# Optimization experiments

Hardware: AMD Instinct MI355X
Metric: run time of the kernel (lower is better)

The kernel has to match this reference:

```python
import jax, jax.numpy as jnp
import numpy as np

NEG = -1e30

def setup_inputs() -> dict:
    key = jax.random.key(0)
    ks = jax.random.split(key, 6)
    B, H, Lc, Lq = 32, 256, 1024, 256
    C = jax.random.normal(ks[0], (B, H, Lc), dtype=jnp.float32)
    Q = jax.random.normal(ks[1], (B, H, Lq), dtype=jnp.float32)
    cmask = jnp.ones((B, Lc), dtype=jnp.int32)
    qmask = jnp.ones((B, Lq), dtype=jnp.int32)
    # xavier_uniform on [3H,1]: bound = sqrt(6/(3H+1))
    bound = float(np.sqrt(6.0 / (3 * H + 1)))
    w = jax.random.uniform(ks[2], (3 * H,), minval=-bound, maxval=bound, dtype=jnp.float32)
    # kaiming_normal (relu, fan_in=4H): std = sqrt(2/(4H))
    W_res = jax.random.normal(ks[3], (H, 4 * H), dtype=jnp.float32) * float(np.sqrt(2.0 / (4 * H)))
    b_res = jnp.zeros((H,), dtype=jnp.float32)
    return {"C": C, "Q": Q, "cmask": cmask, "qmask": qmask, "w": w, "W_res": W_res, "b_res": b_res}

def reference(C, Q, cmask, qmask, w, W_res, b_res):
    H = w.shape[0] // 3
    Ct = jnp.transpose(C, (0, 2, 1))  # [B, Lc, H]
    Qt = jnp.transpose(Q, (0, 2, 1))  # [B, Lq, H]
    w1, w2, w3 = w[:H], w[H:2 * H], w[2 * H:]
    # trilinear similarity S[b,i,j] = Ct_i.w1 + Qt_j.w2 + (Ct_i*Qt_j).w3
    S = (jnp.einsum('blh,h->bl', Ct, w1)[:, :, None]
         + jnp.einsum('bmh,h->bm', Qt, w2)[:, None, :]
         + jnp.einsum('blh,bmh->blm', Ct * w3, Qt))  # [B, Lc, Lq]
    qm = qmask.astype(jnp.float32)[:, None, :]  # [B,1,Lq]
    cm = cmask.astype(jnp.float32)[:, :, None]  # [B,Lc,1]
    S_row = jax.nn.softmax(S + NEG * (1.0 - qm), axis=2)   # over questions
    S_col = jax.nn.softmax(S + NEG * (1.0 - cm), axis=1)   # over context
    A = jnp.einsum('blm,bmh->blh', S_row, Qt)  # [B, Lc, H]
    Bm = jnp.einsum('blm,bkm->blk', S_row, S_col)  # [B, Lc, Lc]
    Bv = jnp.einsum('blk,bkh->blh', Bm, Ct)  # [B, Lc, H]
    cat = jnp.concatenate([Ct, A, Ct * A, Ct * Bv], axis=2)  # [B, Lc, 4H]
    out = jax.nn.relu(jnp.einsum('blf,hf->blh', cat, W_res) + b_res)
    return jnp.transpose(out, (0, 2, 1))  # [B, H, Lc]
```

## Files before the change

### kernel.cpp

```cpp
#include <hip/hip_runtime.h>
#include <math.h>

#define NB 32
#define NH 256
#define NLC 1024
#define NLQ 256
#define NEGV (-1e30f)
#define LCHUNK 16
#define KSPLIT 4

typedef short short8 __attribute__((ext_vector_type(8)));
typedef float f32x4 __attribute__((ext_vector_type(4)));

__device__ inline short bf16_of(float f) {
  union { float f; unsigned u; } v;
  v.f = f;
  unsigned r = (v.u + 0x7fffu + ((v.u >> 16) & 1u)) >> 16;
  return (short)r;
}
__device__ inline float f_of(short s) {
  union { unsigned u; float f; } v;
  v.u = ((unsigned)(unsigned short)s) << 16;
  return v.f;
}
__device__ inline short8 cvt8(float4 a, float4 b) {
  short8 o;
  o[0] = bf16_of(a.x); o[1] = bf16_of(a.y); o[2] = bf16_of(a.z); o[3] = bf16_of(a.w);
  o[4] = bf16_of(b.x); o[5] = bf16_of(b.y); o[6] = bf16_of(b.z); o[7] = bf16_of(b.w);
  return o;
}

__device__ inline void lds_w8(short* lds, int r, int c, short8 v) {
  int byteoff = (r << 6) + (((c ^ ((r >> 1) & 3)) & 3) << 4);
  *(short8*)((char*)lds + byteoff) = v;
}
__device__ inline short8 lds_r8(const short* lds, int R, int g) {
  int byteoff = (R << 6) + (((g ^ ((R >> 1) & 3)) & 3) << 4);
  return *(const short8*)((const char*)lds + byteoff);
}
__device__ inline void stage_g(const short* src, int ld, short* lds, int t) {
  int L = t & 63, w = t >> 6;
  int cp = (L & 3) ^ ((L >> 3) & 3);
#pragma unroll
  for (int i = 0; i < 2; ++i) {
    int seg = w + i * 4;
    const short* g = src + (size_t)(seg * 16 + (L >> 2)) * ld + cp * 8;
    __builtin_amdgcn_global_load_lds(
        (const __attribute__((address_space(1))) unsigned int*)g,
        (__attribute__((address_space(3))) unsigned int*)(lds + seg * 512), 16,
        0, 0);
  }
}

#define GEMM_IDS                                       \
  int t = threadIdx.x, lane = t & 63, w = t >> 6;      \
  int ln = lane & 15, g = lane >> 4;                   \
  int wr = (w >> 1) << 6, wc = (w & 1) << 6;           \
  (void)wr; (void)wc;

#define MFMA_STEP(AS, BS)                                                      \
  {                                                                            \
    short8 af[4], bfr[4];                                                      \
    _Pragma("unroll") for (int mi = 0; mi < 4; ++mi) af[mi] =                  \
        lds_r8(AS, wr + mi * 16 + ln, g);                                      \
    _Pragma("unroll") for (int ni = 0; ni < 4; ++ni) bfr[ni] =                 \
        lds_r8(BS, wc + ni * 16 + ln, g);                                      \
    _Pragma("unroll") for (int mi = 0; mi < 4; ++mi)                           \
        _Pragma("unroll") for (int ni = 0; ni < 4; ++ni) acc[mi][ni] =         \
            __builtin_amdgcn_mfma_f32_16x16x32_bf16(af[mi], bfr[ni],           \
                                                    acc[mi][ni], 0, 0, 0);     \
  }

__global__ __launch_bounds__(256) void k_prep_c(const float* __restrict__ C,
                                                const float* __restrict__ w,
                                                short* __restrict__ Ct_lh,
                                                float* __restrict__ s1p) {
  __shared__ float Ts[64][65];
  __shared__ float red[4][64];
  int b = blockIdx.z, h0 = blockIdx.y << 6, l0 = blockIdx.x << 6;
  int t = threadIdx.x;
  int hr = t >> 4, lc = (t & 15) << 2;
  const float* Cb = C + ((size_t)b * NH + h0) * NLC + l0;
#pragma unroll
  for (int i = 0; i < 4; ++i) {
    float4 v = *(const float4*)&Cb[(size_t)(hr + i * 16) * NLC + lc];
    Ts[hr + i * 16][lc + 0] = v.x;
    Ts[hr + i * 16][lc + 1] = v.y;
    Ts[hr + i * 16][lc + 2] = v.z;
    Ts[hr + i * 16][lc + 3] = v.w;
  }
  __syncthreads();
  int lr = t >> 2, hc = (t & 3) << 4;
  short* dst = &Ct_lh[((size_t)b * NLC + l0 + lr) * NH + h0 + hc];
  short8 o0, o1;
#pragma unroll
  for (int j = 0; j < 8; ++j) o0[j] = bf16_of(Ts[hc + j][lr]);
#pragma unroll
  for (int j = 0; j < 8; ++j) o1[j] = bf16_of(Ts[hc + 8 + j][lr]);
  *(short8*)dst = o0;
  *(short8*)(dst + 8) = o1;
  int q = t >> 6, lq = t & 63;
  float a = 0.f;
#pragma unroll
  for (int j = 0; j < 16; ++j) a += Ts[(q << 4) + j][lq] * w[h0 + (q << 4) + j];
  red[q][lq] = a;
  __syncthreads();
  if (q == 0)
    s1p[((size_t)blockIdx.y * NB + b) * NLC + l0 + lq] =
        red[0][lq] + red[1][lq] + red[2][lq] + red[3][lq];
}

__global__ __launch_bounds__(256) void k_prep_q(const float* __restrict__ Q,
                                                const float* __restrict__ w,
                                                short* __restrict__ Qtw3,
                                                short* __restrict__ Qb_hm,
                                                float* __restrict__ s2p) {
  __shared__ float Ts[64][65];
  __shared__ float red[4][64];
  int b = blockIdx.z, h0 = blockIdx.y << 6, m0 = blockIdx.x << 6;
  int t = threadIdx.x;
  int hr = t >> 4, mc = (t & 15) << 2;
  const float* w3 = w + 2 * NH;
  const float* Qb = Q + ((size_t)b * NH + h0) * NLQ + m0;
#pragma unroll
  for (int i = 0; i < 4; ++i) {
    int h = hr + i * 16;
    float w3v = w3[h0 + h];
    float4 v = *(const float4*)&Qb[(size_t)h * NLQ + mc];
    short4 qb;
    qb.x = bf16_of(v.x); qb.y = bf16_of(v.y);
    qb.z = bf16_of(v.z); qb.w = bf16_of(v.w);
    *(short4*)&Qb_hm[((size_t)b * NH + h0 + h) * NLQ + m0 + mc] = qb;
    Ts[h][mc + 0] = v.x * w3v;
    Ts[h][mc + 1] = v.y * w3v;
    Ts[h][mc + 2] = v.z * w3v;
    Ts[h][mc + 3] = v.w * w3v;
  }
  __syncthreads();
  int mr = t >> 2, hc = (t & 3) << 4;
  short* dst = &Qtw3[((size_t)b * NLQ + m0 + mr) * NH + h0 + hc];
  short8 o0, o1;
#pragma unroll
  for (int j = 0; j < 8; ++j) o0[j] = bf16_of(Ts[hc + j][mr]);
#pragma unroll
  for (int j = 0; j < 8; ++j) o1[j] = bf16_of(Ts[hc + 8 + j][mr]);
  *(short8*)dst = o0;
  *(short8*)(dst + 8) = o1;
  int q = t >> 6, mq = t & 63;
  const float* w2 = w + NH;
  float a = 0.f;
#pragma unroll
  for (int j = 0; j < 16; ++j) {
    int h = (q << 4) + j;
    a += Qb[(size_t)h * NLQ + mq] * w2[h0 + h];
  }
  red[q][mq] = a;
  __syncthreads();
  if (q == 0)
    s2p[((size_t)blockIdx.y * NB + b) * NLQ + m0 + mq] =
        red[0][mq] + red[1][mq] + red[2][mq] + red[3][mq];
}

__global__ __launch_bounds__(256) void k_sfin(const float* __restrict__ s1p,
                                              const float* __restrict__ s2p,
                                              float* __restrict__ s1,
                                              float* __restrict__ s2) {
  int i = blockIdx.x * 256 + threadIdx.x;
  const int N1 = NB * NLC, N2 = NB * NLQ;
  if (i < N1) {
    s1[i] = s1p[i] + s1p[N1 + i] + s1p[2 * N1 + i] + s1p[3 * N1 + i];
  } else {
    int j = i - N1;
    s2[j] = s2p[j] + s2p[N2 + j] + s2p[2 * N2 + j] + s2p[3 * N2 + j];
  }
}

__global__ __launch_bounds__(256) void k_prep_bf16(const float* __restrict__ X,
                                                   short* __restrict__ Y) {
  size_t i = ((size_t)blockIdx.x * 256 + threadIdx.x) * 8;
  float4 v0 = *(const float4*)&X[i];
  float4 v1 = *(const float4*)&X[i + 4];
  *(short8*)&Y[i] = cvt8(v0, v1);
}

__global__ __launch_bounds__(256) void k_sgemm(
    const short* __restrict__ Ct_lh, const short* __restrict__ Qtw3,
    const float* __restrict__ s1, const float* __restrict__ s2,
    float* __restrict__ S) {
  __shared__ short As[2][4096], Bs[2][4096];
  int b = blockIdx.z, l0 = blockIdx.y << 7, m0 = blockIdx.x << 7;
  GEMM_IDS
  const short* Ag = Ct_lh + ((size_t)b * NLC + l0) * NH;
  const short* Bg = Qtw3 + ((size_t)b * NLQ + m0) * NH;
  f32x4 acc[4][4] = {};
  stage_g(Ag, NH, As[0], t);
  stage_g(Bg, NH, Bs[0], t);
  __syncthreads();
  int cur = 0;
  for (int kn = 32; kn <= NH; kn += 32) {
    if (kn < NH) {
      stage_g(Ag + kn, NH, As[cur ^ 1], t);
      stage_g(Bg + kn, NH, Bs[cur ^ 1], t);
    }
    MFMA_STEP(As[cur], Bs[cur])
    __syncthreads();
    cur ^= 1;
  }
#pragma unroll
  for (int mi = 0; mi < 4; ++mi)
#pragma unroll
    for (int ni = 0; ni < 4; ++ni)
#pragma unroll
      for (int r = 0; r < 4; ++r) {
        int l = l0 + wr + mi * 16 + g * 4 + r;
        int m = m0 + wc + ni * 16 + ln;
        S[((size_t)b * NLC + l) * NLQ + m] =
            acc[mi][ni][r] + s1[b * NLC + l] + s2[b * NLQ + m];
      }
}

__global__ __launch_bounds__(256) void k_colpart(const float* __restrict__ S,
                                                 const int* __restrict__ cmask,
                                                 float* __restrict__ pmax,
                                                 float* __restrict__ psum) {
  int idx = blockIdx.x;
  int chunk = idx & (LCHUNK - 1);
  int mb = (idx >> 4) & 3;
  int b = idx >> 6;
  int m0 = mb << 6;
  int tx = threadIdx.x & 63, ty = threadIdx.x >> 6;
  const float* Sb = S + (size_t)b * NLC * NLQ + (size_t)(chunk * 64) * NLQ;
  const int* cm = cmask + b * NLC + chunk * 64;
  float mx = -INFINITY, sm = 0.f;
#pragma unroll 4
  for (int l = ty; l < 64; l += 4) {
    float x = Sb[(size_t)l * NLQ + m0 + tx] + (cm[l] ? 0.f : NEGV);
    float nmx = fmaxf(mx, x);
    sm = sm * expf(mx - nmx) + expf(x - nmx);
    mx = nmx;
  }
  __shared__ float smx[4][64], ssm[4][64];
  smx[ty][tx] = mx;
  ssm[ty][tx] = sm;
  __syncthreads();
  if (ty == 0) {
#pragma unroll
    for (int r = 1; r < 4; ++r) {
      float m2 = smx[r][tx], s2 = ssm[r][tx];
      float nm = fmaxf(mx, m2);
      sm = sm * expf(mx - nm) + s2 * expf(m2 - nm);
      mx = nm;
    }
    int m = (b << 8) + m0 + tx;
    pmax[(size_t)m * LCHUNK + chunk] = mx;
    psum[(size_t)m * LCHUNK + chunk] = sm;
  }
}

__global__ __launch_bounds__(256) void k_colfin(const float* __restrict__ pmax,
                                                const float* __restrict__ psum,
                                                float* __restrict__ cmax,
                                                float* __restrict__ cinv) {
  int m = blockIdx.x * 256 + threadIdx.x;
  const float* pm = pmax + (size_t)m * LCHUNK;
  const float* ps = psum + (size_t)m * LCHUNK;
  float mx = pm[0], sm = ps[0];
#pragma unroll
  for (int c = 1; c < LCHUNK; ++c) {
    float m2 = pm[c], s2 = ps[c];
    float nm = fmaxf(mx, m2);
    sm = sm * expf(mx - nm) + s2 * expf(m2 - nm);
    mx = nm;
  }
  cmax[m] = mx;
  cinv[m] = 1.0f / sm;
}

__global__ __launch_bounds__(256) void k_rowsoft(float* __restrict__ S,
                                                 const int* __restrict__ qmask,
                                                 const int* __restrict__ cmask,
                                                 const float* __restrict__ cmax,
                                                 const float* __restrict__ cinv) {
  int wave = threadIdx.x >> 6, lane = threadIdx.x & 63;
  int idx = (blockIdx.x << 2) + wave;
  int b = idx >> 10;
  float* row = S + (size_t)idx * NLQ;
  const int* qm = qmask + b * NLQ;
  int m4 = lane << 2;
  float4 v = *(const float4*)&row[m4];
  int4 q = *(const int4*)&qm[m4];
  float x0 = v.x + (q.x ? 0.f : NEGV);
  float x1 = v.y + (q.y ? 0.f : NEGV);
  float x2 = v.z + (q.z ? 0.f : NEGV);
  float x3 = v.w + (q.w ? 0.f : NEGV);
  float mx = fmaxf(fmaxf(x0, x1), fmaxf(x2, x3));
#pragma unroll
  for (int off = 32; off > 0; off >>= 1) mx = fmaxf(mx, __shfl_xor(mx, off));
  float p0 = expf(x0 - mx), p1 = expf(x1 - mx);
  float p2 = expf(x2 - mx), p3 = expf(x3 - mx);
  float sm = p0 + p1 + p2 + p3;
#pragma unroll
  for (int off = 32; off > 0; off >>= 1) sm += __shfl_xor(sm, off);
  float iv = 1.0f / sm;
  short4 o;
  o.x = bf16_of(p0 * iv);
  o.y = bf16_of(p1 * iv);
  o.z = bf16_of(p2 * iv);
  o.w = bf16_of(p3 * iv);
  float cmf = (float)cmask[idx];
  float4 cm4 = *(const float4*)&cmax[(b << 8) + m4];
  float4 ci4 = *(const float4*)&cinv[(b << 8) + m4];
  short4 oc;
  oc.x = bf16_of(expf(v.x - cm4.x) * ci4.x * cmf);
  oc.y = bf16_of(expf(v.y - cm4.y) * ci4.y * cmf);
  oc.z = bf16_of(expf(v.z - cm4.z) * ci4.z * cmf);
  oc.w = bf16_of(expf(v.w - cm4.w) * ci4.w * cmf);
  *(short4*)((short*)row + m4) = o;
  *(short4*)((short*)row + 256 + m4) = oc;
}

__global__ __launch_bounds__(256) void k_tgemm(const float* __restrict__ C,
                                               const short* __restrict__ PcolS,
                                               float* __restrict__ Tp) {
  __shared__ short As[4096], Bs[4096];
  int b = blockIdx.z;
  int ks = blockIdx.y;
  int h0 = (blockIdx.x & 1) << 7;
  int m0 = (blockIdx.x >> 1) << 7;
  GEMM_IDS
  const float* Cb = C + ((size_t)b * NH + h0) * NLC;
  const short* Pb = PcolS + (size_t)b * NLC * 512 + 256 + m0;
  f32x4 acc[4][4] = {};
  int kbeg = ks * (NLC / KSPLIT), kend = kbeg + NLC / KSPLIT;
  int ca = lane & 3;
  int lloc = t >> 3, g2 = lloc >> 3, kin = lloc & 7;
  int mbase = (t & 7) << 4;
  for (int k0 = kbeg; k0 < kend; k0 += 32) {
    __syncthreads();
    {
#pragma unroll
      for (int i = 0; i < 2; ++i) {
        int seg = w + i * 4, r = seg * 16 + (lane >> 2);
        const float* src = &Cb[(size_t)r * NLC + k0 + ca * 8];
        float4 v0 = *(const float4*)src;
        float4 v1 = *(const float4*)(src + 4);
        lds_w8(As, r, ca, cvt8(v0, v1));
      }
    }
    {
      const short* srow = Pb + (size_t)(k0 + lloc) * 512;
      short8 x0 = *(const short8*)&srow[mbase];
      short8 x1 = *(const short8*)&srow[mbase + 8];
#pragma unroll
      for (int j = 0; j < 8; ++j) {
        int R = mbase + j;
        int byteoff =
            (R << 6) + (((g2 ^ ((R >> 1) & 3)) & 3) << 4) + (kin << 1);
        *(short*)((char*)Bs + byteoff) = x0[j];
      }
#pragma unroll
      for (int j = 0; j < 8; ++j) {
        int R = mbase + 8 + j;
        int byteoff =
            (R << 6) + (((g2 ^ ((R >> 1) & 3)) & 3) << 4) + (kin << 1);
        *(short*)((char*)Bs + byteoff) = x1[j];
      }
    }
    __syncthreads();
    MFMA_STEP(As, Bs)
  }
  float* dst = Tp + ((size_t)ks * NB + b) * NH * NLQ;
#pragma unroll
  for (int mi = 0; mi < 4; ++mi)
#pragma unroll
    for (int ni = 0; ni < 4; ++ni)
#pragma unroll
      for (int r = 0; r < 4; ++r) {
        int h = h0 + wr + mi * 16 + g * 4 + r;
        int m = m0 + wc + ni * 16 + ln;
        dst[(size_t)h * NLQ + m] = acc[mi][ni][r];
      }
}

__global__ __launch_bounds__(256) void k_tfin(const float* __restrict__ Tp,
                                              short* __restrict__ Tt) {
  size_t i = ((size_t)blockIdx.x * 256 + threadIdx.x) * 4;
  const size_t stride = (size_t)NB * NH * NLQ;
  float4 s = *(const float4*)&Tp[i];
#pragma unroll
  for (int ks = 1; ks < KSPLIT; ++ks) {
    float4 v = *(const float4*)&Tp[i + ks * stride];
    s.x += v.x; s.y += v.y; s.z += v.z; s.w += v.w;
  }
  short4 o;
  o.x = bf16_of(s.x);
  o.y = bf16_of(s.y);
  o.z = bf16_of(s.z);
  o.w = bf16_of(s.w);
  *(short4*)&Tt[i] = o;
}

__global__ __launch_bounds__(256) void k_abgemm(
    const short* __restrict__ Prow, const short* __restrict__ Qb_hm,
    const short* __restrict__ Tt, const short* __restrict__ Ct_lh,
    short* __restrict__ A_lh, short* __restrict__ CtBv_lh) {
  __shared__ short As[2][4096], Bs[2][4096];
  int b = blockIdx.z, l0 = blockIdx.y << 7, nb = blockIdx.x;
  GEMM_IDS
  const short* Ag = Prow + ((size_t)b * NLC + l0) * 512;
  const short* Bbase = (nb < 2)
                           ? Qb_hm + ((size_t)b * NH + nb * 128) * NLQ
                           : Tt + ((size_t)b * NH + (nb - 2) * 128) * NLQ;
  f32x4 acc[4][4] = {};
  stage_g(Ag, 512, As[0], t);
  stage_g(Bbase, NLQ, Bs[0], t);
  __syncthreads();
  int cur = 0;
  for (int kn = 32; kn <= NLQ; kn += 32) {
    if (kn < NLQ) {
      stage_g(Ag + kn, 512, As[cur ^ 1], t);
      stage_g(Bbase + kn, NLQ, Bs[cur ^ 1], t);
    }
    MFMA_STEP(As[cur], Bs[cur])
    __syncthreads();
    cur ^= 1;
  }
  int hbase = (nb & 1) << 7;
  if (nb < 2) {
#pragma unroll
    for (int mi = 0; mi < 4; ++mi)
#pragma unroll
      for (int ni = 0; ni < 4; ++ni)
#pragma unroll
        for (int r = 0; r < 4; ++r) {
          int l = l0 + wr + mi * 16 + g * 4 + r;
          int h = hbase + wc + ni * 16 + ln;
          A_lh[((size_t)b * NLC + l) * NH + h] = bf16_of(acc[mi][ni][r]);
        }
  } else {
#pragma unroll
    for (int mi = 0; mi < 4; ++mi)
#pragma unroll
      for (int ni = 0; ni < 4; ++ni)
#pragma unroll
        for (int r = 0; r < 4; ++r) {
          int l = l0 + wr + mi * 16 + g * 4 + r;
          int h = hbase + wc + ni * 16 + ln;
          size_t off = ((size_t)b * NLC + l) * NH + h;
          CtBv_lh[off] = bf16_of(f_of(Ct_lh[off]) * acc[mi][ni][r]);
        }
  }
}

__global__ __launch_bounds__(256) void k_out(
    const short* __restrict__ Wb, const short* __restrict__ Ct_lh,
    const short* __restrict__ A_lh, const short* __restrict__ CtBv_lh,
    const float* __restrict__ br, float* __restrict__ out) {
  __shared__ short As[2][4096], Bs[2][4096];
  int b = blockIdx.z, h0 = blockIdx.y << 7, l0 = blockIdx.x << 7;
  GEMM_IDS
  const short* Wg = Wb + (size_t)h0 * (4 * NH);
  size_t boff = ((size_t)b * NLC + l0) * NH;
  f32x4 acc[4][4] = {};
  stage_g(Wg, 4 * NH, As[0], t);
  stage_g(Ct_lh + boff, NH, Bs[0], t);
  __syncthreads();
  int cur = 0;
  for (int kn = 32; kn <= 4 * NH; kn += 32) {
    bool has = kn < 4 * NH;
    int regn = kn >> 8, kon = kn & 255;
    short8 x1[2], x2[2];
    int ca = lane & 3;
    if (has) {
      stage_g(Wg + kn, 4 * NH, As[cur ^ 1], t);
      if (regn != 2) {
        const short* base = (regn == 0) ? Ct_lh : (regn == 1) ? A_lh : CtBv_lh;
        stage_g(base + boff + kon, NH, Bs[cur ^ 1], t);
      } else {
#pragma unroll
        for (int i = 0; i < 2; ++i) {
          int seg = w + i * 4, r = seg * 16 + (lane >> 2);
          size_t off = boff + (size_t)r * NH + kon + ca * 8;
          x1[i] = *(const short8*)&Ct_lh[off];
          x2[i] = *(const short8*)&A_lh[off];
        }
      }
    }
    MFMA_STEP(As[cur], Bs[cur])
    if (has && regn == 2) {
#pragma unroll
      for (int i = 0; i < 2; ++i) {
        int seg = w + i * 4, r = seg * 16 + (lane >> 2);
        short8 o;
#pragma unroll
        for (int j = 0; j < 8; ++j)
          o[j] = bf16_of(f_of(x1[i][j]) * f_of(x2[i][j]));
        lds_w8(Bs[cur ^ 1], r, ca, o);
      }
    }
    __syncthreads();
    cur ^= 1;
  }
#pragma unroll
  for (int mi = 0; mi < 4; ++mi)
#pragma unroll
    for (int ni = 0; ni < 4; ++ni) {
      int h = h0 + wr + mi * 16 + g * 4;
      int l = l0 + wc + ni * 16 + ln;
#pragma unroll
      for (int r = 0; r < 4; ++r) {
        float bias = br[h + r];
        out[((size_t)b * NH + h + r) * NLC + l] =
            fmaxf(acc[mi][ni][r] + bias, 0.f);
      }
    }
}

extern "C" void kernel_launch(void* const* d_in, const int* in_sizes, int n_in,
                              void* d_out, int out_size, void* d_ws,
                              size_t ws_size, hipStream_t stream) {
  (void)in_sizes;
  (void)n_in;
  (void)out_size;
  (void)ws_size;
  const float* C = (const float*)d_in[0];
  const float* Q = (const float*)d_in[1];
  const int* cmask = (const int*)d_in[2];
  const int* qmask = (const int*)d_in[3];
  const float* w = (const float*)d_in[4];
  const float* W = (const float*)d_in[5];
  const float* br = (const float*)d_in[6];
  float* out = (float*)d_out;

  char* p = (char*)d_ws;
  float* S = (float*)p;       p += (size_t)NB * NLC * NLQ * 4;
  short* Ct_lh = (short*)p;   p += (size_t)NB * NLC * NH * 2;
  short* A_lh = (short*)p;    p += (size_t)NB * NLC * NH * 2;
  short* CtBv_lh = (short*)p; p += (size_t)NB * NLC * NH * 2;
  short* Tt = (short*)p;      p += (size_t)NB * NH * NLQ * 2;
  short* Qtw3 = (short*)p;    p += (size_t)NB * NLQ * NH * 2;
  short* Qb_hm = (short*)p;   p += (size_t)NB * NH * NLQ * 2;
  short* Wb = (short*)p;      p += (size_t)NH * 4 * NH * 2;
  float* s1 = (float*)p;      p += (size_t)NB * NLC * 4;
  float* s2 = (float*)p;      p += (size_t)NB * NLQ * 4;
  float* cmax = (float*)p;    p += (size_t)NB * NLQ * 4;
  float* cinv = (float*)p;    p += (size_t)NB * NLQ * 4;
  float* pmax = (float*)p;    p += (size_t)NB * NLQ * LCHUNK * 4;
  float* psum = (float*)p;    p += (size_t)NB * NLQ * LCHUNK * 4;
  float* s1p = (float*)p;     p += (size_t)4 * NB * NLC * 4;
  float* s2p = (float*)p;     p += (size_t)4 * NB * NLQ * 4;
  float* Tp = (float*)A_lh;
  short* Prow = (short*)S;

  k_prep_c<<<dim3(NLC / 64, NH / 64, NB), dim3(256), 0, stream>>>(C, w, Ct_lh,
                                                                  s1p);
  k_prep_q<<<dim3(NLQ / 64, NH / 64, NB), dim3(256), 0, stream>>>(
      Q, w, Qtw3, Qb_hm, s2p);
  k_prep_bf16<<<dim3(NH * 4 * NH / 2048), dim3(256), 0, stream>>>(W, Wb);
  k_sfin<<<dim3((NB * NLC + NB * NLQ) / 256), dim3(256), 0, stream>>>(
      s1p, s2p, s1, s2);
  k_sgemm<<<dim3(NLQ / 128, NLC / 128, NB), dim3(256), 0, stream>>>(
      Ct_lh, Qtw3, s1, s2, S);
  k_colpart<<<dim3(NB * 4 * LCHUNK), dim3(256), 0, stream>>>(S, cmask, pmax,
                                                             psum);
  k_colfin<<<dim3(NB * NLQ / 256), dim3(256), 0, stream>>>(pmax, psum, cmax,
                                                           cinv);
  k_rowsoft<<<dim3(NB * NLC / 4), dim3(256), 0, stream>>>(S, qmask, cmask,
                                                          cmax, cinv);
  k_tgemm<<<dim3(4, KSPLIT, NB), dim3(256), 0, stream>>>(C, Prow, Tp);
  k_tfin<<<dim3(NB * NH * NLQ / 1024), dim3(256), 0, stream>>>(Tp, Tt);
  k_abgemm<<<dim3(4, NLC / 128, NB), dim3(256), 0, stream>>>(
      Prow, Qb_hm, Tt, Ct_lh, A_lh, CtBv_lh);
  k_out<<<dim3(NLC / 128, NH / 128, NB), dim3(256), 0, stream>>>(
      Wb, Ct_lh, A_lh, CtBv_lh, br, out);
}
```

Measured before the change: 153.8 us.

## Fuse column-softmax partials into S GEMM epilogue and pre-convert C to bf16

The S GEMM epilogue now computes per-column max and sum-exp partials for its 128-row tile, using lane shuffles and LDS to combine them. This replaces the separate k_colpart pass that re-read the whole S matrix. k_prep_c also writes an h-major bf16 copy of C so that k_tgemm can stage it with the shared bf16 loader instead of loading fp32 and converting. In exchange the GEMM epilogue gains exp work and extra registers, and a new 16 MB bf16 buffer is written.

```diff
diff --git a/kernel.cpp b/kernel.cpp
--- a/kernel.cpp
+++ b/kernel.cpp
@@ -6,7 +6,7 @@
 #define NLC 1024
 #define NLQ 256
 #define NEGV (-1e30f)
-#define LCHUNK 16
+#define TCH 8
 #define KSPLIT 4
 
 typedef short short8 __attribute__((ext_vector_type(8)));
@@ -74,6 +74,7 @@
 __global__ __launch_bounds__(256) void k_prep_c(const float* __restrict__ C,
                                                 const float* __restrict__ w,
                                                 short* __restrict__ Ct_lh,
+                                                short* __restrict__ Cb_hl,
                                                 float* __restrict__ s1p) {
   __shared__ float Ts[64][65];
   __shared__ float red[4][64];
@@ -83,11 +84,16 @@
   const float* Cb = C + ((size_t)b * NH + h0) * NLC + l0;
 #pragma unroll
   for (int i = 0; i < 4; ++i) {
-    float4 v = *(const float4*)&Cb[(size_t)(hr + i * 16) * NLC + lc];
-    Ts[hr + i * 16][lc + 0] = v.x;
-    Ts[hr + i * 16][lc + 1] = v.y;
-    Ts[hr + i * 16][lc + 2] = v.z;
-    Ts[hr + i * 16][lc + 3] = v.w;
+    int h = hr + i * 16;
+    float4 v = *(const float4*)&Cb[(size_t)h * NLC + lc];
+    short4 cb;
+    cb.x = bf16_of(v.x); cb.y = bf16_of(v.y);
+    cb.z = bf16_of(v.z); cb.w = bf16_of(v.w);
+    *(short4*)&Cb_hl[((size_t)b * NH + h0 + h) * NLC + l0 + lc] = cb;
+    Ts[h][lc + 0] = v.x;
+    Ts[h][lc + 1] = v.y;
+    Ts[h][lc + 2] = v.z;
+    Ts[h][lc + 3] = v.w;
   }
   __syncthreads();
   int lr = t >> 2, hc = (t & 3) << 4;
@@ -186,8 +192,11 @@
 __global__ __launch_bounds__(256) void k_sgemm(
     const short* __restrict__ Ct_lh, const short* __restrict__ Qtw3,
     const float* __restrict__ s1, const float* __restrict__ s2,
-    float* __restrict__ S) {
+    const int* __restrict__ cmask, float* __restrict__ S,
+    float* __restrict__ pmax, float* __restrict__ psum) {
   __shared__ short As[2][4096], Bs[2][4096];
+  __shared__ float cmsh[128];
+  __shared__ float sredm[4][4][16], sreds[4][4][16];
   int b = blockIdx.z, l0 = blockIdx.y << 7, m0 = blockIdx.x << 7;
   GEMM_IDS
   const short* Ag = Ct_lh + ((size_t)b * NLC + l0) * NH;
@@ -206,54 +215,74 @@
     __syncthreads();
     cur ^= 1;
   }
+  if (t < 128) cmsh[t] = cmask[b * NLC + l0 + t] ? 0.f : NEGV;
+  __syncthreads();
+  float s1r[16], ncr[16];
 #pragma unroll
   for (int mi = 0; mi < 4; ++mi)
 #pragma unroll
-    for (int ni = 0; ni < 4; ++ni)
+    for (int r = 0; r < 4; ++r) {
+      int lloc = wr + mi * 16 + g * 4 + r;
+      s1r[mi * 4 + r] = s1[b * NLC + l0 + lloc];
+      ncr[mi * 4 + r] = cmsh[lloc];
+    }
+  float s2v[4], mxc[4], smc[4];
+#pragma unroll
+  for (int ni = 0; ni < 4; ++ni) {
+    s2v[ni] = s2[b * NLQ + m0 + wc + ni * 16 + ln];
+    mxc[ni] = -INFINITY;
+    smc[ni] = 0.f;
+  }
+#pragma unroll
+  for (int ni = 0; ni < 4; ++ni)
+#pragma unroll
+    for (int mi = 0; mi < 4; ++mi)
+#pragma unroll
+      for (int r = 0; r < 4; ++r)
+        mxc[ni] = fmaxf(mxc[ni],
+                        acc[mi][ni][r] + s1r[mi * 4 + r] + s2v[ni] +
+                            ncr[mi * 4 + r]);
+#pragma unroll
+  for (int ni = 0; ni < 4; ++ni) {
+    int m = m0 + wc + ni * 16 + ln;
+#pragma unroll
+    for (int mi = 0; mi < 4; ++mi)
 #pragma unroll
       for (int r = 0; r < 4; ++r) {
         int l = l0 + wr + mi * 16 + g * 4 + r;
-        int m = m0 + wc + ni * 16 + ln;
-        S[((size_t)b * NLC + l) * NLQ + m] =
-            acc[mi][ni][r] + s1[b * NLC + l] + s2[b * NLQ + m];
-      }
-}
-
-__global__ __launch_bounds__(256) void k_colpart(const float* __restrict__ S,
-                                                 const int* __restrict__ cmask,
-                                                 float* __restrict__ pmax,
-                                                 float* __restrict__ psum) {
-  int idx = blockIdx.x;
-  int chunk = idx & (LCHUNK - 1);
-  int mb = (idx >> 4) & 3;
-  int b = idx >> 6;
-  int m0 = mb << 6;
-  int tx = threadIdx.x & 63, ty = threadIdx.x >> 6;
-  const float* Sb = S + (size_t)b * NLC * NLQ + (size_t)(chunk * 64) * NLQ;
-  const int* cm = cmask + b * NLC + chunk * 64;
-  float mx = -INFINITY, sm = 0.f;
-#pragma unroll 4
-  for (int l = ty; l < 64; l += 4) {
-    float x = Sb[(size_t)l * NLQ + m0 + tx] + (cm[l] ? 0.f : NEGV);
-    float nmx = fmaxf(mx, x);
-    sm = sm * expf(mx - nmx) + expf(x - nmx);
-    mx = nmx;
-  }
-  __shared__ float smx[4][64], ssm[4][64];
-  smx[ty][tx] = mx;
-  ssm[ty][tx] = sm;
-  __syncthreads();
-  if (ty == 0) {
-#pragma unroll
-    for (int r = 1; r < 4; ++r) {
-      float m2 = smx[r][tx], s2 = ssm[r][tx];
-      float nm = fmaxf(mx, m2);
-      sm = sm * expf(mx - nm) + s2 * expf(m2 - nm);
-      mx = nm;
-    }
-    int m = (b << 8) + m0 + tx;
-    pmax[(size_t)m * LCHUNK + chunk] = mx;
-    psum[(size_t)m * LCHUNK + chunk] = sm;
+        float sv = acc[mi][ni][r] + s1r[mi * 4 + r] + s2v[ni];
+        S[((size_t)b * NLC + l) * NLQ + m] = sv;
+        smc[ni] += expf(sv + ncr[mi * 4 + r] - mxc[ni]);
+      }
+  }
+#pragma unroll
+  for (int off = 16; off <= 32; off <<= 1)
+#pragma unroll
+    for (int ni = 0; ni < 4; ++ni) {
+      float m2 = __shfl_xor(mxc[ni], off);
+      float s2x = __shfl_xor(smc[ni], off);
+      float nm = fmaxf(mxc[ni], m2);
+      smc[ni] = smc[ni] * expf(mxc[ni] - nm) + s2x * expf(m2 - nm);
+      mxc[ni] = nm;
+    }
+  if (lane < 16) {
+#pragma unroll
+    for (int ni = 0; ni < 4; ++ni) {
+      sredm[w][ni][lane] = mxc[ni];
+      sreds[w][ni][lane] = smc[ni];
+    }
+  }
+  __syncthreads();
+  if (t < 128) {
+    int wcsel = t >> 6, nii = (t >> 4) & 3, lnn = t & 15;
+    float mA = sredm[wcsel][nii][lnn], sA = sreds[wcsel][nii][lnn];
+    float mB = sredm[wcsel + 2][nii][lnn], sB = sreds[wcsel + 2][nii][lnn];
+    float nm = fmaxf(mA, mB);
+    float sm = sA * expf(mA - nm) + sB * expf(mB - nm);
+    int m = m0 + (wcsel << 6) + nii * 16 + lnn;
+    size_t base = ((size_t)b * NLQ + m) * TCH + blockIdx.y;
+    pmax[base] = nm;
+    psum[base] = sm;
   }
 }
 
@@ -262,11 +291,11 @@
                                                 float* __restrict__ cmax,
                                                 float* __restrict__ cinv) {
   int m = blockIdx.x * 256 + threadIdx.x;
-  const float* pm = pmax + (size_t)m * LCHUNK;
-  const float* ps = psum + (size_t)m * LCHUNK;
+  const float* pm = pmax + (size_t)m * TCH;
+  const float* ps = psum + (size_t)m * TCH;
   float mx = pm[0], sm = ps[0];
 #pragma unroll
-  for (int c = 1; c < LCHUNK; ++c) {
+  for (int c = 1; c < TCH; ++c) {
     float m2 = pm[c], s2 = ps[c];
     float nm = fmaxf(mx, m2);
     sm = sm * expf(mx - nm) + s2 * expf(m2 - nm);
@@ -319,7 +348,7 @@
   *(short4*)((short*)row + 256 + m4) = oc;
 }
 
-__global__ __launch_bounds__(256) void k_tgemm(const float* __restrict__ C,
+__global__ __launch_bounds__(256) void k_tgemm(const short* __restrict__ Cb_hl,
                                                const short* __restrict__ PcolS,
                                                float* __restrict__ Tp) {
   __shared__ short As[4096], Bs[4096];
@@ -328,25 +357,15 @@
   int h0 = (blockIdx.x & 1) << 7;
   int m0 = (blockIdx.x >> 1) << 7;
   GEMM_IDS
-  const float* Cb = C + ((size_t)b * NH + h0) * NLC;
+  const short* Ag = Cb_hl + ((size_t)b * NH + h0) * NLC;
   const short* Pb = PcolS + (size_t)b * NLC * 512 + 256 + m0;
   f32x4 acc[4][4] = {};
   int kbeg = ks * (NLC / KSPLIT), kend = kbeg + NLC / KSPLIT;
-  int ca = lane & 3;
   int lloc = t >> 3, g2 = lloc >> 3, kin = lloc & 7;
   int mbase = (t & 7) << 4;
   for (int k0 = kbeg; k0 < kend; k0 += 32) {
     __syncthreads();
-    {
-#pragma unroll
-      for (int i = 0; i < 2; ++i) {
-        int seg = w + i * 4, r = seg * 16 + (lane >> 2);
-        const float* src = &Cb[(size_t)r * NLC + k0 + ca * 8];
-        float4 v0 = *(const float4*)src;
-        float4 v1 = *(const float4*)(src + 4);
-        lds_w8(As, r, ca, cvt8(v0, v1));
-      }
-    }
+    stage_g(Ag + k0, NLC, As, t);
     {
       const short* srow = Pb + (size_t)(k0 + lloc) * 512;
       short8 x0 = *(const short8*)&srow[mbase];
@@ -537,6 +556,7 @@
   short* Ct_lh = (short*)p;   p += (size_t)NB * NLC * NH * 2;
   short* A_lh = (short*)p;    p += (size_t)NB * NLC * NH * 2;
   short* CtBv_lh = (short*)p; p += (size_t)NB * NLC * NH * 2;
+  short* Cb_hl = (short*)p;   p += (size_t)NB * NH * NLC * 2;
   short* Tt = (short*)p;      p += (size_t)NB * NH * NLQ * 2;
   short* Qtw3 = (short*)p;    p += (size_t)NB * NLQ * NH * 2;
   short* Qb_hm = (short*)p;   p += (size_t)NB * NH * NLQ * 2;
@@ -545,29 +565,27 @@
   float* s2 = (float*)p;      p += (size_t)NB * NLQ * 4;
   float* cmax = (float*)p;    p += (size_t)NB * NLQ * 4;
   float* cinv = (float*)p;    p += (size_t)NB * NLQ * 4;
-  float* pmax = (float*)p;    p += (size_t)NB * NLQ * LCHUNK * 4;
-  float* psum = (float*)p;    p += (size_t)NB * NLQ * LCHUNK * 4;
+  float* pmax = (float*)p;    p += (size_t)NB * NLQ * TCH * 4;
+  float* psum = (float*)p;    p += (size_t)NB * NLQ * TCH * 4;
   float* s1p = (float*)p;     p += (size_t)4 * NB * NLC * 4;
   float* s2p = (float*)p;     p += (size_t)4 * NB * NLQ * 4;
   float* Tp = (float*)A_lh;
   short* Prow = (short*)S;
 
   k_prep_c<<<dim3(NLC / 64, NH / 64, NB), dim3(256), 0, stream>>>(C, w, Ct_lh,
-                                                                  s1p);
+                                                                  Cb_hl, s1p);
   k_prep_q<<<dim3(NLQ / 64, NH / 64, NB), dim3(256), 0, stream>>>(
       Q, w, Qtw3, Qb_hm, s2p);
   k_prep_bf16<<<dim3(NH * 4 * NH / 2048), dim3(256), 0, stream>>>(W, Wb);
   k_sfin<<<dim3((NB * NLC + NB * NLQ) / 256), dim3(256), 0, stream>>>(
       s1p, s2p, s1, s2);
   k_sgemm<<<dim3(NLQ / 128, NLC / 128, NB), dim3(256), 0, stream>>>(
-      Ct_lh, Qtw3, s1, s2, S);
-  k_colpart<<<dim3(NB * 4 * LCHUNK), dim3(256), 0, stream>>>(S, cmask, pmax,
-                                                             psum);
+      Ct_lh, Qtw3, s1, s2, cmask, S, pmax, psum);
   k_colfin<<<dim3(NB * NLQ / 256), dim3(256), 0, stream>>>(pmax, psum, cmax,
                                                            cinv);
   k_rowsoft<<<dim3(NB * NLC / 4), dim3(256), 0, stream>>>(S, qmask, cmask,
                                                           cmax, cinv);
-  k_tgemm<<<dim3(4, KSPLIT, NB), dim3(256), 0, stream>>>(C, Prow, Tp);
+  k_tgemm<<<dim3(4, KSPLIT, NB), dim3(256), 0, stream>>>(Cb_hl, Prow, Tp);
   k_tfin<<<dim3(NB * NH * NLQ / 1024), dim3(256), 0, stream>>>(Tp, Tt);
   k_abgemm<<<dim3(4, NLC / 128, NB), dim3(256), 0, stream>>>(
       Prow, Qb_hm, Tt, Ct_lh, A_lh, CtBv_lh);
```

After: 146.0 us. -5.1%, faster.
